# Kernel tuning notes

Hardware: AMD Instinct MI355X
Metric: run time of the kernel (lower is better)

## Reference

```python
import jax, jax.numpy as jnp
import numpy as np

EPS = 1e-8

def setup_inputs() -> dict:
    key = jax.random.key(0)
    k1, k2, k3, k4 = jax.random.split(key, 4)
    x_cnn = jax.random.normal(k1, (8, 256, 128, 128), dtype=jnp.float32)
    x_vit = jax.random.normal(k2, (8, 512, 32, 32), dtype=jnp.float32)
    W = jax.random.normal(k3, (256, 512), dtype=jnp.float32) * 0.05  # 1x1 conv weight
    b = jax.random.normal(k4, (256,), dtype=jnp.float32) * 0.05
    return {"x_cnn": x_cnn, "x_vit": x_vit, "W": W, "b": b}

def reference(x_cnn, x_vit, W, b):
    # 1x1 conv projection: 512 -> cnn_channels
    v = jnp.einsum('oc,bchw->bohw', W, x_vit) + b[None, :, None, None]
    B, C, H, Wd = x_cnn.shape
    if v.shape[2:] != (H, Wd):
        # bilinear, half-pixel centers == torch align_corners=False
        v = jax.image.resize(v, (B, C, H, Wd), method='bilinear')
    # Per-pixel cosine similarity over channels. The original computes a full
    # (HW x HW) bmm and keeps only the diagonal; the diagonal equals this
    # per-pixel channel dot product, so the math is identical.
    dot = jnp.sum(x_cnn * v, axis=1)               # [B,H,W]
    n_cnn = jnp.sqrt(jnp.sum(x_cnn * x_cnn, axis=1))
    n_vit = jnp.sqrt(jnp.sum(v * v, axis=1))
    sim = dot / (n_cnn * n_vit + EPS)
    return sim[:, None, :, :]                      # [B,1,H,W]
```

## Files before the change

### kernel.cpp

```cpp
#include <hip/hip_runtime.h>
#include <hip/hip_bf16.h>

typedef __attribute__((ext_vector_type(8))) short bf16x8;
typedef __attribute__((ext_vector_type(4))) float f32x4;
typedef __attribute__((ext_vector_type(8))) unsigned short u16x8;

static __device__ __forceinline__ unsigned short f2bf(float f) {
    union { float f; unsigned int u; } v; v.f = f;
    unsigned int u = v.u;
    u += 0x7FFFu + ((u >> 16) & 1u);
    return (unsigned short)(u >> 16);
}

__global__ void __launch_bounds__(256) convert_w(const float* __restrict__ W,
                                                 unsigned short* __restrict__ Wbf) {
    int i = (blockIdx.x * 256 + threadIdx.x) * 4;
    float4 v = *(const float4*)(W + i);
    ushort4 o;
    o.x = f2bf(v.x); o.y = f2bf(v.y); o.z = f2bf(v.z); o.w = f2bf(v.w);
    *(ushort4*)(Wbf + i) = o;
}

__global__ void __launch_bounds__(256) transpose_xvit(const float* __restrict__ X,
                                                      unsigned short* __restrict__ Xt) {
    __shared__ unsigned short ls[64][65];
    int b  = blockIdx.z;
    int c0 = blockIdx.y * 64;
    int p0 = blockIdx.x * 64;
    int t  = threadIdx.x;

    const float* src = X + ((size_t)b * 512 + c0) * 1024 + p0;
    int cc = t >> 4;
    int p4 = (t & 15) << 2;
    #pragma unroll
    for (int i = 0; i < 4; ++i) {
        int c = cc + i * 16;
        float4 v = *(const float4*)(src + (size_t)c * 1024 + p4);
        ls[p4 + 0][c] = f2bf(v.x);
        ls[p4 + 1][c] = f2bf(v.y);
        ls[p4 + 2][c] = f2bf(v.z);
        ls[p4 + 3][c] = f2bf(v.w);
    }
    __syncthreads();

    unsigned short* dst = Xt + ((size_t)b * 1024 + p0) * 512 + c0;
    int pp  = t >> 2;
    int c16 = (t & 3) << 4;
    u16x8 w0, w1;
    #pragma unroll
    for (int j = 0; j < 8; ++j) { w0[j] = ls[pp][c16 + j]; w1[j] = ls[pp][c16 + 8 + j]; }
    *(u16x8*)(dst + (size_t)pp * 512 + c16)     = w0;
    *(u16x8*)(dst + (size_t)pp * 512 + c16 + 8) = w1;
}

__global__ void __launch_bounds__(256) gemm_bf16(const unsigned short* __restrict__ Wbf,
                                                 const unsigned short* __restrict__ Xt,
                                                 const float* __restrict__ bias,
                                                 float* __restrict__ V) {
    __shared__ __align__(16) unsigned short As[64 * 32];
    __shared__ __align__(16) unsigned short Bs[64 * 32];

    int b  = blockIdx.z;
    int m0 = blockIdx.y * 64;
    int n0 = blockIdx.x * 64;
    int t  = threadIdx.x;
    int wave = t >> 6;
    int lane = t & 63;
    int wm = (wave >> 1) * 32;
    int wn = (wave & 1) * 32;
    int l15  = lane & 15;
    int quad = lane >> 4;

    const unsigned short* Aglob = Wbf + (size_t)(m0 + (t >> 2)) * 512 + ((t & 3) << 3);
    const unsigned short* Bglob = Xt + ((size_t)b * 1024 + n0 + (t >> 2)) * 512 + ((t & 3) << 3);
    unsigned short* Asw = As + (t >> 2) * 32 + ((t & 3) << 3);
    unsigned short* Bsw = Bs + (t >> 2) * 32 + ((t & 3) << 3);

    f32x4 acc[2][2] = {};

    for (int k0 = 0; k0 < 512; k0 += 32) {
        *(u16x8*)Asw = *(const u16x8*)(Aglob + k0);
        *(u16x8*)Bsw = *(const u16x8*)(Bglob + k0);
        __syncthreads();

        bf16x8 a0 = *(const bf16x8*)(As + (wm + l15) * 32 + quad * 8);
        bf16x8 a1 = *(const bf16x8*)(As + (wm + 16 + l15) * 32 + quad * 8);
        bf16x8 b0 = *(const bf16x8*)(Bs + (wn + l15) * 32 + quad * 8);
        bf16x8 b1 = *(const bf16x8*)(Bs + (wn + 16 + l15) * 32 + quad * 8);

        acc[0][0] = __builtin_amdgcn_mfma_f32_16x16x32_bf16(a0, b0, acc[0][0], 0, 0, 0);
        acc[0][1] = __builtin_amdgcn_mfma_f32_16x16x32_bf16(a0, b1, acc[0][1], 0, 0, 0);
        acc[1][0] = __builtin_amdgcn_mfma_f32_16x16x32_bf16(a1, b0, acc[1][0], 0, 0, 0);
        acc[1][1] = __builtin_amdgcn_mfma_f32_16x16x32_bf16(a1, b1, acc[1][1], 0, 0, 0);
        __syncthreads();
    }

    #pragma unroll
    for (int mi = 0; mi < 2; ++mi)
        #pragma unroll
        for (int ni = 0; ni < 2; ++ni)
            #pragma unroll
            for (int r = 0; r < 4; ++r) {
                int gm = m0 + wm + mi * 16 + quad * 4 + r;
                int gn = n0 + wn + ni * 16 + l15;
                V[((size_t)b * 256 + gm) * 1024 + gn] = acc[mi][ni][r] + bias[gm];
            }
}

__global__ void __launch_bounds__(256) fused_cos(const float* __restrict__ xcnn,
                                                 const float* __restrict__ V,
                                                 float* __restrict__ out) {
    int g  = blockIdx.x * 256 + threadIdx.x;
    int b  = g >> 14;
    int hw = g & 16383;
    int h  = hw >> 7;
    int w  = hw & 127;

    float sy = (h + 0.5f) * 0.25f - 0.5f;
    float sx = (w + 0.5f) * 0.25f - 0.5f;
    float fy = floorf(sy), fx = floorf(sx);
    float dy = sy - fy,   dx = sx - fx;
    int y0 = max(0, min(31, (int)fy));
    int y1 = max(0, min(31, (int)fy + 1));
    int x0 = max(0, min(31, (int)fx));
    int x1 = max(0, min(31, (int)fx + 1));
    float w00 = (1.f - dy) * (1.f - dx);
    float w01 = (1.f - dy) * dx;
    float w10 = dy * (1.f - dx);
    float w11 = dy * dx;

    const float* xc = xcnn + (size_t)b * 256 * 16384 + hw;
    const float* vb = V + (size_t)b * 256 * 1024;
    int o00 = y0 * 32 + x0, o01 = y0 * 32 + x1;
    int o10 = y1 * 32 + x0, o11 = y1 * 32 + x1;

    float dot = 0.f, nx = 0.f, nv = 0.f;
    #pragma unroll 4
    for (int c = 0; c < 256; ++c) {
        float xv = xc[(size_t)c * 16384];
        const float* vc = vb + c * 1024;
        float v = w00 * vc[o00] + w01 * vc[o01] + w10 * vc[o10] + w11 * vc[o11];
        dot += xv * v;
        nx  += xv * xv;
        nv  += v * v;
    }
    out[g] = dot / (sqrtf(nx) * sqrtf(nv) + 1e-8f);
}

extern "C" void kernel_launch(void* const* d_in, const int* in_sizes, int n_in,
                              void* d_out, int out_size, void* d_ws, size_t ws_size,
                              hipStream_t stream) {
    const float* x_cnn = (const float*)d_in[0];
    const float* x_vit = (const float*)d_in[1];
    const float* W     = (const float*)d_in[2];
    const float* bias  = (const float*)d_in[3];
    float* out = (float*)d_out;

    char* ws = (char*)d_ws;
    float*          V   = (float*)ws;
    unsigned short* Xt  = (unsigned short*)(ws + 8388608);
    unsigned short* Wbf = (unsigned short*)(ws + 16777216);

    convert_w<<<128, 256, 0, stream>>>(W, Wbf);
    transpose_xvit<<<dim3(16, 8, 8), 256, 0, stream>>>(x_vit, Xt);
    gemm_bf16<<<dim3(16, 4, 8), 256, 0, stream>>>(Wbf, Xt, bias, V);
    fused_cos<<<512, 256, 0, stream>>>(x_cnn, V, out);
}
```

Baseline: 232.4 us.

## Restructure cosine kernel: split channels across warps, vectorize pixels, reduce in LDS

The fused cosine kernel now uses one block per (batch,row). Each 32-lane group handles a 32-channel slice, and each thread covers 4 adjacent pixels with float4 loads of x_cnn. The bilinear interpolation is factored into a vertical blend of 4 contiguous V values plus per-pixel horizontal weights, which cuts redundant gathers. Partial dot products and norms are reduced across the 8 channel slices through shared memory. The grid doubles so more blocks are in flight on the bandwidth-bound pass over x_cnn, at the cost of an LDS reduction and a barrier.

```diff
diff --git a/kernel.cpp b/kernel.cpp
--- a/kernel.cpp
+++ b/kernel.cpp
@@ -4,6 +4,7 @@
 typedef __attribute__((ext_vector_type(8))) short bf16x8;
 typedef __attribute__((ext_vector_type(4))) float f32x4;
 typedef __attribute__((ext_vector_type(8))) unsigned short u16x8;
+typedef __attribute__((ext_vector_type(4), aligned(4))) float f32x4u;
 
 static __device__ __forceinline__ unsigned short f2bf(float f) {
     union { float f; unsigned int u; } v; v.f = f;
@@ -110,41 +111,89 @@
 __global__ void __launch_bounds__(256) fused_cos(const float* __restrict__ xcnn,
                                                  const float* __restrict__ V,
                                                  float* __restrict__ out) {
-    int g  = blockIdx.x * 256 + threadIdx.x;
-    int b  = g >> 14;
-    int hw = g & 16383;
-    int h  = hw >> 7;
-    int w  = hw & 127;
+    __shared__ float red[8 * 385];
+
+    int bh = blockIdx.x;
+    int b  = bh >> 7;
+    int h  = bh & 127;
+    int t  = threadIdx.x;
+    int q  = t & 31;
+    int cs = t >> 5;
 
     float sy = (h + 0.5f) * 0.25f - 0.5f;
-    float sx = (w + 0.5f) * 0.25f - 0.5f;
-    float fy = floorf(sy), fx = floorf(sx);
-    float dy = sy - fy,   dx = sx - fx;
+    float fy = floorf(sy);
+    float dy = sy - fy;
     int y0 = max(0, min(31, (int)fy));
     int y1 = max(0, min(31, (int)fy + 1));
-    int x0 = max(0, min(31, (int)fx));
-    int x1 = max(0, min(31, (int)fx + 1));
-    float w00 = (1.f - dy) * (1.f - dx);
-    float w01 = (1.f - dy) * dx;
-    float w10 = dy * (1.f - dx);
-    float w11 = dy * dx;
-
-    const float* xc = xcnn + (size_t)b * 256 * 16384 + hw;
-    const float* vb = V + (size_t)b * 256 * 1024;
-    int o00 = y0 * 32 + x0, o01 = y0 * 32 + x1;
-    int o10 = y1 * 32 + x0, o11 = y1 * 32 + x1;
-
-    float dot = 0.f, nx = 0.f, nv = 0.f;
-    #pragma unroll 4
-    for (int c = 0; c < 256; ++c) {
-        float xv = xc[(size_t)c * 16384];
-        const float* vc = vb + c * 1024;
-        float v = w00 * vc[o00] + w01 * vc[o01] + w10 * vc[o10] + w11 * vc[o11];
-        dot += xv * v;
-        nx  += xv * xv;
-        nv  += v * v;
-    }
-    out[g] = dot / (sqrtf(nx) * sqrtf(nv) + 1e-8f);
+
+    int cb = max(0, min(28, q - 1));
+    float a[4][4];
+    #pragma unroll
+    for (int px = 0; px < 4; ++px) {
+        #pragma unroll
+        for (int j = 0; j < 4; ++j) a[px][j] = 0.f;
+        int w = q * 4 + px;
+        float sx = (w + 0.5f) * 0.25f - 0.5f;
+        float fx = floorf(sx);
+        float dx = sx - fx;
+        int x0 = max(0, min(31, (int)fx));
+        int x1 = max(0, min(31, (int)fx + 1));
+        a[px][x0 - cb] += 1.f - dx;
+        a[px][x1 - cb] += dx;
+    }
+
+    const float* xp = xcnn + ((size_t)(b * 256 + cs * 32) * 16384) + h * 128 + q * 4;
+    const float* vt = V + ((size_t)(b * 256 + cs * 32) * 1024) + y0 * 32 + cb;
+    const float* vb = V + ((size_t)(b * 256 + cs * 32) * 1024) + y1 * 32 + cb;
+    float ry = dy, ry0 = 1.f - dy;
+
+    float dot[4] = {0.f, 0.f, 0.f, 0.f};
+    float nx [4] = {0.f, 0.f, 0.f, 0.f};
+    float nv [4] = {0.f, 0.f, 0.f, 0.f};
+
+    #pragma unroll 8
+    for (int c = 0; c < 32; ++c) {
+        float4  xv  = *(const float4*)(xp + (size_t)c * 16384);
+        f32x4u  top = *(const f32x4u*)(vt + (size_t)c * 1024);
+        f32x4u  bot = *(const f32x4u*)(vb + (size_t)c * 1024);
+        float bl0 = ry0 * top[0] + ry * bot[0];
+        float bl1 = ry0 * top[1] + ry * bot[1];
+        float bl2 = ry0 * top[2] + ry * bot[2];
+        float bl3 = ry0 * top[3] + ry * bot[3];
+        float xs[4] = {xv.x, xv.y, xv.z, xv.w};
+        #pragma unroll
+        for (int px = 0; px < 4; ++px) {
+            float v = a[px][0] * bl0 + a[px][1] * bl1 + a[px][2] * bl2 + a[px][3] * bl3;
+            dot[px] += xs[px] * v;
+            nx [px] += xs[px] * xs[px];
+            nv [px] += v * v;
+        }
+    }
+
+    float* my = red + cs * 385;
+    #pragma unroll
+    for (int px = 0; px < 4; ++px) {
+        int o = (q * 4 + px) * 3;
+        my[o + 0] = dot[px];
+        my[o + 1] = nx[px];
+        my[o + 2] = nv[px];
+    }
+    __syncthreads();
+
+    if (t < 128) {
+        int px = t & 3;
+        int q2 = t >> 2;
+        int o  = (q2 * 4 + px) * 3;
+        float d = 0.f, sx2 = 0.f, sv2 = 0.f;
+        #pragma unroll
+        for (int s = 0; s < 8; ++s) {
+            d   += red[s * 385 + o + 0];
+            sx2 += red[s * 385 + o + 1];
+            sv2 += red[s * 385 + o + 2];
+        }
+        out[(size_t)b * 16384 + h * 128 + q2 * 4 + px] =
+            d / (sqrtf(sx2) * sqrtf(sv2) + 1e-8f);
+    }
 }
 
 extern "C" void kernel_launch(void* const* d_in, const int* in_sizes, int n_in,
@@ -164,5 +213,5 @@
     convert_w<<<128, 256, 0, stream>>>(W, Wbf);
     transpose_xvit<<<dim3(16, 8, 8), 256, 0, stream>>>(x_vit, Xt);
     gemm_bf16<<<dim3(16, 4, 8), 256, 0, stream>>>(Wbf, Xt, bias, V);
-    fused_cos<<<512, 256, 0, stream>>>(x_cnn, V, out);
-}
+    fused_cos<<<1024, 256, 0, stream>>>(x_cnn, V, out);
+}
```

After: 223.1 us. 1.04x faster.
